# Performance work log

Measured on AMD Instinct MI355X. Metric: run time of the kernel, lower is better.

## Reference

```python
import jax, jax.numpy as jnp
import numpy as np
import math

M, INPUT_DIM, CLASSES, LATENT = 4096, 64, 10, 2

# ---- Bessel-approximation phi functions (Abramowitz & Stegun polynomial series) ----

def phi_f(s):
    t = s / 7.5
    t2 = t * t
    poly = 1.0 + 3.5156229 * t2 + 3.0899424 * t2**2 + 1.2067492 * t2**3 \
         + 0.2659732 * t2**4 + 0.0360768 * t2**5 + 0.0045813 * t2**6
    return jnp.exp(-s / 2.0) * poly


def phi_g(s):
    t = s / 7.5
    u = 1.0 / t  # s >= 7.5 when called via phi, so t >= 1
    poly = 0.39894228 + 0.01328592 * u + 0.00225319 * u**2 - 0.00157565 * u**3 \
         + 0.0091628 * u**4 - 0.02057706 * u**5 + 0.02635537 * u**6 \
         - 0.01647633 * u**7 + 0.00392377 * u**8
    return jnp.sqrt(2.0 / s) * poly


def phi(x):
    a = jnp.float32(7.5)
    return phi_f(jnp.minimum(x, a)) - phi_f(a) + phi_g(jnp.maximum(x, a))


def phi_d(s, D):
    if D <= 2:
        return phi(s)
    return 1.0 / jnp.sqrt(1.0 + 4.0 * s / (2 * D - 3))


def cramer_wold_distance(X, mu, variance, p, gamma):
    m, K = X.shape
    variance_matrix = variance[None, :] + variance[:, None]          # [C, C]
    # A term: pairwise latent-sample distances [m, m]
    A1 = jnp.sum((X[None, :, :] - X[:, None, :]) ** 2, axis=-1)      # [m, m]
    A = jnp.sum(phi_d(A1 / (4.0 * gamma), K)) / (m * m * math.sqrt(2.0 * math.pi * 2.0 * gamma))
    # B term: sample-to-mean distances [m, C]
    B1 = jnp.sum((mu[None, :, :] - X[:, None, :]) ** 2, axis=-1)     # [m, C]
    B2 = phi_d(B1 / (2.0 * (variance + 2.0 * gamma)), K)
    B = jnp.sum(2.0 * p / (m * jnp.sqrt(2.0 * math.pi * (variance + 2.0 * gamma))) * B2)
    # C term: mean-to-mean distances [C, C]
    C1 = jnp.sum((mu[None, :, :] - mu[:, None, :]) ** 2, axis=-1)
    C2 = phi_d(C1 / (2.0 * variance_matrix + 4.0 * gamma), K)
    C3 = jnp.outer(p, p) / jnp.sqrt(2.0 * math.pi * (variance_matrix + 2.0 * gamma))
    C = jnp.sum(C3 * C2)
    return A - B + C


def setup_inputs() -> dict:
    key = jax.random.key(0)
    ks = jax.random.split(key, 12)
    tau = jax.random.normal(ks[0], (M, INPUT_DIM), dtype=jnp.float32)
    # first half of batch is labeled (one-hot), second half unlabeled (zeros)
    lab_idx = jax.random.randint(ks[1], (M // 2,), 0, CLASSES)
    labels = jnp.concatenate([jax.nn.one_hot(lab_idx, CLASSES, dtype=jnp.float32),
                              jnp.zeros((M - M // 2, CLASSES), jnp.float32)], axis=0)
    batch_data = jnp.concatenate([tau, labels], axis=1)

    def xavier(k, fan_in, fan_out):
        lim = math.sqrt(6.0 / (fan_in + fan_out))
        return jax.random.uniform(k, (fan_in, fan_out), jnp.float32, -lim, lim)

    inp = {
        'batch_data': batch_data,
        'We1': xavier(ks[2], INPUT_DIM, 32), 'be1': jnp.zeros((32,), jnp.float32),
        'We2': xavier(ks[3], 32, 16),        'be2': jnp.zeros((16,), jnp.float32),
        'We3': xavier(ks[4], 16, LATENT),    'be3': jnp.zeros((LATENT,), jnp.float32),
        'Wd1': xavier(ks[5], LATENT, 16),    'bd1': jnp.zeros((16,), jnp.float32),
        'Wd2': xavier(ks[6], 16, 32),        'bd2': jnp.zeros((32,), jnp.float32),
        'Wd3': xavier(ks[7], 32, INPUT_DIM), 'bd3': jnp.zeros((INPUT_DIM,), jnp.float32),
        # GMM: init=2.0, gauss_num <= z_dim branch not taken (10 > 2) -> N(0, init)
        'means': 2.0 * jax.random.normal(ks[8], (CLASSES, LATENT), jnp.float32),
        'variances': jnp.ones((CLASSES,), jnp.float32),
        'probs': jnp.full((CLASSES,), 1.0 / CLASSES, jnp.float32),
    }
    return inp


def segma_forward(batch_data, We1, be1, We2, be2, We3, be3,
                  Wd1, bd1, Wd2, bd2, Wd3, bd3, means, variances, probs):
    tau = batch_data[:, :INPUT_DIM]
    labels = batch_data[:, INPUT_DIM:]
    # encoder
    x = jnp.tanh(tau @ We1 + be1)
    x = jnp.tanh(x @ We2 + be2)
    z = x @ We3 + be3                                               # [m, K]
    # decoder
    h = jnp.tanh(z @ Wd1 + bd1)
    h = jnp.tanh(h @ Wd2 + bd2)
    tau_decoded = h @ Wd3 + bd3
    rec_loss = jnp.mean((tau - tau_decoded) ** 2)
    # labeled mask: rows whose one-hot labels sum to exactly 1
    labeled_mask = (jnp.sum(labels, axis=-1) == 1.0)
    # class logits: Gaussian log-likelihood under each mixture component
    D = means.shape[-1]
    sq = jnp.sum((z[:, None, :] - means[None, :, :]) ** 2, axis=-1)  # [m, C]
    class_logits = jnp.log(probs) - 0.5 * D * jnp.log(2.0 * math.pi * variances) - sq / (2.0 * variances)
    # cross-entropy with (soft/one-hot) float targets, masked to labeled rows
    ce = -jnp.sum(labels * jax.nn.log_softmax(class_logits, axis=-1), axis=-1)
    den = jnp.sum(labels)
    den = jnp.where(den == 0, 1.0, den)
    class_loss = jnp.sum(ce * labeled_mask.astype(jnp.float32)) / den
    # Cramer-Wold cost (train_labeled=True -> use all z)
    m = z.shape[0]
    gamma = jnp.float32((4.0 / (3.0 * m)) ** 0.2)
    cw_cost = cramer_wold_distance(z, means, variances, probs, gamma)
    log_cw_cost = 8.0 + jnp.log(cw_cost)
    total_loss = rec_loss + 1.0 * log_cw_cost + 2.0 * class_loss
    return total_loss


def reference(batch_data, We1, be1, We2, be2, We3, be3,
              Wd1, bd1, Wd2, bd2, Wd3, bd3, means, variances, probs):
    return segma_forward(batch_data, We1, be1, We2, be2, We3, be3,
                         Wd1, bd1, Wd2, bd2, Wd3, bd3, means, variances, probs)
```

## Files before the change

kernel.cpp:

```cpp
#include <hip/hip_runtime.h>
#include <math.h>

#define M_ROWS 4096
#define IN_DIM 64
#define NCLS 10
#define ROW_STRIDE 74
#define TWO_PI_F 6.283185307179586f

__device__ __forceinline__ float phi_f_eval(float s) {
    float t = s * (1.0f / 7.5f);
    float t2 = t * t;
    float p = 0.0045813f;
    p = fmaf(p, t2, 0.0360768f);
    p = fmaf(p, t2, 0.2659732f);
    p = fmaf(p, t2, 1.2067492f);
    p = fmaf(p, t2, 3.0899424f);
    p = fmaf(p, t2, 3.5156229f);
    p = fmaf(p, t2, 1.0f);
    return __expf(-0.5f * s) * p;
}

__device__ __forceinline__ float phi_g_eval(float s) {
    float r = __builtin_amdgcn_rcpf(s);
    float u = 7.5f * r;
    float p = 0.00392377f;
    p = fmaf(p, u, -0.01647633f);
    p = fmaf(p, u, 0.02635537f);
    p = fmaf(p, u, -0.02057706f);
    p = fmaf(p, u, 0.0091628f);
    p = fmaf(p, u, -0.00157565f);
    p = fmaf(p, u, 0.00225319f);
    p = fmaf(p, u, 0.01328592f);
    p = fmaf(p, u, 0.39894228f);
    return __builtin_amdgcn_sqrtf(2.0f * r) * p;
}

#define PHI_F_75 0.21445709f

__device__ __forceinline__ float phi_eval(float s) {
    float f = phi_f_eval(fminf(s, 7.5f));
    float g = phi_g_eval(fmaxf(s, 7.5f));
    return f - PHI_F_75 + g;
}

__device__ __forceinline__ float fast_tanh(float x) {
    float e = __expf(2.0f * x);
    float r = __builtin_amdgcn_rcpf(e + 1.0f);
    return fmaf(-2.0f, r, 1.0f);
}

__device__ __forceinline__ float waveReduce(float v) {
    v += __shfl_down(v, 32, 64);
    v += __shfl_down(v, 16, 64);
    v += __shfl_down(v, 8, 64);
    v += __shfl_down(v, 4, 64);
    v += __shfl_down(v, 2, 64);
    v += __shfl_down(v, 1, 64);
    return v;
}

#define O_W1T   0
#define O_W2T   2048
#define O_WD2T  2560
#define O_WD3T  3072
#define O_W3T   5120
#define O_WD1T  5152
#define O_B1    5184
#define O_B2    5216
#define O_B3    5232
#define O_BD1   5236
#define O_BD2   5252
#define O_BD3   5284
#define O_MU    5348
#define O_VAR   5368
#define O_PRB   5378
#define SM_TOT  5392

__global__ __launch_bounds__(64, 1) void k_mlp(
    const float* __restrict__ batch,
    const float* __restrict__ We1, const float* __restrict__ be1,
    const float* __restrict__ We2, const float* __restrict__ be2,
    const float* __restrict__ We3, const float* __restrict__ be3,
    const float* __restrict__ Wd1, const float* __restrict__ bd1,
    const float* __restrict__ Wd2, const float* __restrict__ bd2,
    const float* __restrict__ Wd3, const float* __restrict__ bd3,
    const float* __restrict__ means, const float* __restrict__ vars,
    const float* __restrict__ probs,
    float2* __restrict__ zbuf,
    float* __restrict__ recp, float* __restrict__ Bp,
    float* __restrict__ clsp, float* __restrict__ labp,
    float gamma)
{
    __shared__ __align__(16) float sm[SM_TOT];
    const int tid = threadIdx.x;

    for (int idx = tid; idx < 2048; idx += 64) { int i = idx >> 5, j = idx & 31; sm[O_W1T + j * 64 + i] = We1[idx]; }
    for (int idx = tid; idx < 512;  idx += 64) { int i = idx >> 4, j = idx & 15; sm[O_W2T + j * 32 + i] = We2[idx]; }
    for (int idx = tid; idx < 512;  idx += 64) { int i = idx >> 5, j = idx & 31; sm[O_WD2T + j * 16 + i] = Wd2[idx]; }
    for (int idx = tid; idx < 2048; idx += 64) { int i = idx >> 6, j = idx & 63; sm[O_WD3T + j * 32 + i] = Wd3[idx]; }
    if (tid < 32) { int i = tid >> 1, j = tid & 1;  sm[O_W3T + j * 16 + i] = We3[tid]; }
    else          { int t2 = tid - 32; int i = t2 >> 4, j = t2 & 15; sm[O_WD1T + j * 2 + i] = Wd1[t2]; }
    if (tid < 32) sm[O_B1 + tid] = be1[tid];
    if (tid < 16) sm[O_B2 + tid] = be2[tid];
    if (tid < 2)  sm[O_B3 + tid] = be3[tid];
    if (tid < 16) sm[O_BD1 + tid] = bd1[tid];
    if (tid < 32) sm[O_BD2 + tid] = bd2[tid];
    {
        sm[O_BD3 + tid] = bd3[tid];
    }
    if (tid < 20) sm[O_MU + tid] = means[tid];
    if (tid < 10) sm[O_VAR + tid] = vars[tid];
    if (tid < 10) sm[O_PRB + tid] = probs[tid];
    __syncthreads();

    const int row = blockIdx.x * 64 + tid;
    const float* rp = batch + (size_t)row * ROW_STRIDE;

    float tau[64];
#pragma unroll
    for (int i = 0; i < 32; i++) {
        float2 v = ((const float2*)rp)[i];
        tau[2 * i] = v.x; tau[2 * i + 1] = v.y;
    }

    float x1[32];
#pragma unroll
    for (int j = 0; j < 32; j++) {
        const float4* w = (const float4*)&sm[O_W1T + j * 64];
        float acc = sm[O_B1 + j];
#pragma unroll
        for (int i = 0; i < 16; i++) {
            float4 wv = w[i];
            acc = fmaf(tau[4 * i],     wv.x, acc);
            acc = fmaf(tau[4 * i + 1], wv.y, acc);
            acc = fmaf(tau[4 * i + 2], wv.z, acc);
            acc = fmaf(tau[4 * i + 3], wv.w, acc);
        }
        x1[j] = fast_tanh(acc);
    }

    float x2[16];
#pragma unroll
    for (int j = 0; j < 16; j++) {
        const float4* w = (const float4*)&sm[O_W2T + j * 32];
        float acc = sm[O_B2 + j];
#pragma unroll
        for (int i = 0; i < 8; i++) {
            float4 wv = w[i];
            acc = fmaf(x1[4 * i],     wv.x, acc);
            acc = fmaf(x1[4 * i + 1], wv.y, acc);
            acc = fmaf(x1[4 * i + 2], wv.z, acc);
            acc = fmaf(x1[4 * i + 3], wv.w, acc);
        }
        x2[j] = fast_tanh(acc);
    }

    float z0 = sm[O_B3 + 0], z1 = sm[O_B3 + 1];
#pragma unroll
    for (int i = 0; i < 16; i++) {
        z0 = fmaf(x2[i], sm[O_W3T + 0 * 16 + i], z0);
        z1 = fmaf(x2[i], sm[O_W3T + 1 * 16 + i], z1);
    }
    zbuf[row] = make_float2(z0, z1);

    float h1[16];
#pragma unroll
    for (int j = 0; j < 16; j++) {
        float acc = sm[O_BD1 + j];
        acc = fmaf(z0, sm[O_WD1T + j * 2 + 0], acc);
        acc = fmaf(z1, sm[O_WD1T + j * 2 + 1], acc);
        h1[j] = fast_tanh(acc);
    }

    float h2[32];
#pragma unroll
    for (int j = 0; j < 32; j++) {
        const float4* w = (const float4*)&sm[O_WD2T + j * 16];
        float acc = sm[O_BD2 + j];
#pragma unroll
        for (int i = 0; i < 4; i++) {
            float4 wv = w[i];
            acc = fmaf(h1[4 * i],     wv.x, acc);
            acc = fmaf(h1[4 * i + 1], wv.y, acc);
            acc = fmaf(h1[4 * i + 2], wv.z, acc);
            acc = fmaf(h1[4 * i + 3], wv.w, acc);
        }
        h2[j] = fast_tanh(acc);
    }

    float rec = 0.0f;
#pragma unroll
    for (int o = 0; o < 64; o++) {
        const float4* w = (const float4*)&sm[O_WD3T + o * 32];
        float acc = sm[O_BD3 + o];
#pragma unroll
        for (int i = 0; i < 8; i++) {
            float4 wv = w[i];
            acc = fmaf(h2[4 * i],     wv.x, acc);
            acc = fmaf(h2[4 * i + 1], wv.y, acc);
            acc = fmaf(h2[4 * i + 2], wv.z, acc);
            acc = fmaf(h2[4 * i + 3], wv.w, acc);
        }
        float e = acc - tau[o];
        rec = fmaf(e, e, rec);
    }

    const float two_g = 2.0f * gamma;
    const float inv_m = 1.0f / (float)M_ROWS;
    float lg[NCLS];
    float mx = -3.0e38f;
    float Bacc = 0.0f;
#pragma unroll
    for (int c = 0; c < NCLS; c++) {
        float d0 = z0 - sm[O_MU + 2 * c];
        float d1 = z1 - sm[O_MU + 2 * c + 1];
        float sqc = fmaf(d0, d0, d1 * d1);
        float vc = sm[O_VAR + c];
        float lgc = __logf(sm[O_PRB + c]) - __logf(TWO_PI_F * vc)
                    - sqc * 0.5f * __builtin_amdgcn_rcpf(vc);
        lg[c] = lgc;
        mx = fmaxf(mx, lgc);

        float den = vc + two_g;
        float sB = sqc * 0.5f * __builtin_amdgcn_rcpf(den);
        float coef = 2.0f * inv_m * sm[O_PRB + c] * __builtin_amdgcn_rsqf(TWO_PI_F * den);
        Bacc = fmaf(coef, phi_eval(sB), Bacc);
    }
    float esum = 0.0f;
#pragma unroll
    for (int c = 0; c < NCLS; c++) esum += __expf(lg[c] - mx);
    float lse = __logf(esum) + mx;

    float suml = 0.0f, ce = 0.0f;
#pragma unroll
    for (int c = 0; c < NCLS; c++) {
        float lb = rp[IN_DIM + c];
        suml += lb;
        ce = fmaf(lb, lse - lg[c], ce);
    }
    float cls = (suml == 1.0f) ? ce : 0.0f;

    float r0 = waveReduce(rec);
    float r1 = waveReduce(Bacc);
    float r2 = waveReduce(cls);
    float r3 = waveReduce(suml);
    if (tid == 0) {
        recp[blockIdx.x] = r0;
        Bp[blockIdx.x]   = r1;
        clsp[blockIdx.x] = r2;
        labp[blockIdx.x] = r3;
    }
}

__global__ __launch_bounds__(64, 1) void k_pair(
    const float2* __restrict__ z, float* __restrict__ Apart, float inv4g)
{
    const int ti = blockIdx.x, tj = blockIdx.y;
    const int bid = blockIdx.x + gridDim.x * blockIdx.y;
    const int lane = threadIdx.x;
    if (tj < ti) {
        if (lane == 0) Apart[bid] = 0.0f;
        return;
    }
    __shared__ float2 zjs[64];
    const int i = ti * 64 + lane;
    float2 zi = z[i];
    zjs[lane] = z[tj * 64 + lane];
    __syncthreads();

    const bool offd = (ti != tj);
    float acc = 0.0f;
#pragma unroll 8
    for (int jj = 0; jj < 64; jj++) {
        float dx = zi.x - zjs[jj].x;
        float dy = zi.y - zjs[jj].y;
        float s = fmaf(dx, dx, dy * dy) * inv4g;
        float p = phi_eval(s);
        if (offd || (tj * 64 + jj) > i) acc += p;
    }
    float tot = waveReduce(acc);
    if (lane == 0) Apart[bid] = tot;
}

__global__ __launch_bounds__(256) void k_fin(
    const float* __restrict__ means, const float* __restrict__ vars,
    const float* __restrict__ probs,
    const float* __restrict__ Apart,
    const float* __restrict__ recp, const float* __restrict__ Bp,
    const float* __restrict__ clsp, const float* __restrict__ labp,
    float* __restrict__ out, float gamma)
{
    __shared__ double sA[256];
    __shared__ double s4[256];
    __shared__ float cbuf[256];
    const int t = threadIdx.x;

    float cval = 0.0f;
    if (t < 100) {
        int ci = t / 10, cj = t - 10 * (t / 10);
        float vm = vars[ci] + vars[cj];
        float d0 = means[2 * ci] - means[2 * cj];
        float d1 = means[2 * ci + 1] - means[2 * cj + 1];
        float c1 = fmaf(d0, d0, d1 * d1);
        float s = c1 / (2.0f * vm + 4.0f * gamma);
        float c2 = phi_eval(s);
        float c3 = probs[ci] * probs[cj] * __builtin_amdgcn_rsqf(TWO_PI_F * (vm + 2.0f * gamma));
        cval = c3 * c2;
    }
    cbuf[t] = cval;

    double av = 0.0;
#pragma unroll
    for (int k = 0; k < 16; k++) av += (double)Apart[t + 256 * k];
    sA[t] = av;

    double pv;
    if (t < 64)       pv = (double)recp[t];
    else if (t < 128) pv = (double)Bp[t - 64];
    else if (t < 192) pv = (double)clsp[t - 128];
    else              pv = (double)labp[t - 192];
    s4[t] = pv;
    __syncthreads();

    if (t == 0) {
        double Asum = 0.0, C = 0.0, rec = 0.0, B = 0.0, cls = 0.0, lab = 0.0;
        for (int k = 0; k < 256; k++) Asum += sA[k];
        for (int k = 0; k < 256; k++) C += (double)cbuf[k];
        for (int k = 0; k < 64; k++)  rec += s4[k];
        for (int k = 64; k < 128; k++) B += s4[k];
        for (int k = 128; k < 192; k++) cls += s4[k];
        for (int k = 192; k < 256; k++) lab += s4[k];

        const double m = (double)M_ROWS;
        const double gam = (double)gamma;
        double phi0 = (double)phi_eval(0.0f);
        double Atot = 2.0 * Asum + m * phi0;
        double A = Atot / (m * m * sqrt(2.0 * M_PI * 2.0 * gam));
        double den = lab; if (den == 0.0) den = 1.0;
        double cw = A - B + C;
        double total = rec / (m * 64.0) + 8.0 + log(cw) + 2.0 * (cls / den);
        out[0] = (float)total;
    }
}

extern "C" void kernel_launch(void* const* d_in, const int* in_sizes, int n_in,
                              void* d_out, int out_size, void* d_ws, size_t ws_size,
                              hipStream_t stream) {
    (void)in_sizes; (void)n_in; (void)out_size; (void)ws_size;
    const float* batch = (const float*)d_in[0];
    const float* We1 = (const float*)d_in[1];
    const float* be1 = (const float*)d_in[2];
    const float* We2 = (const float*)d_in[3];
    const float* be2 = (const float*)d_in[4];
    const float* We3 = (const float*)d_in[5];
    const float* be3 = (const float*)d_in[6];
    const float* Wd1 = (const float*)d_in[7];
    const float* bd1 = (const float*)d_in[8];
    const float* Wd2 = (const float*)d_in[9];
    const float* bd2 = (const float*)d_in[10];
    const float* Wd3 = (const float*)d_in[11];
    const float* bd3 = (const float*)d_in[12];
    const float* means = (const float*)d_in[13];
    const float* vars = (const float*)d_in[14];
    const float* probs = (const float*)d_in[15];

    float* ws = (float*)d_ws;
    float2* zbuf = (float2*)ws;
    float* Apart = ws + 8192;
    float* recp  = ws + 12288;
    float* Bp    = ws + 12352;
    float* clsp  = ws + 12416;
    float* labp  = ws + 12480;

    const float gamma = (float)pow(4.0 / (3.0 * (double)M_ROWS), 0.2);
    const float inv4g = 1.0f / (4.0f * gamma);

    k_mlp<<<64, 64, 0, stream>>>(batch, We1, be1, We2, be2, We3, be3,
                                 Wd1, bd1, Wd2, bd2, Wd3, bd3,
                                 means, vars, probs,
                                 zbuf, recp, Bp, clsp, labp, gamma);
    k_pair<<<dim3(64, 64), 64, 0, stream>>>(zbuf, Apart, inv4g);
    k_fin<<<1, 256, 0, stream>>>(means, vars, probs, Apart, recp, Bp, clsp, labp,
                                 (float*)d_out, gamma);
}
```

Measured before the change: 140.7 us.

## Launch only upper-triangular pair tiles and parallelize final reduction with wave shuffles

```diff
diff --git a/kernel.cpp b/kernel.cpp
--- a/kernel.cpp
+++ b/kernel.cpp
@@ -6,6 +6,8 @@
 #define NCLS 10
 #define ROW_STRIDE 74
 #define TWO_PI_F 6.283185307179586f
+#define NTILE 64
+#define NPAIR 2080
 
 __device__ __forceinline__ float phi_f_eval(float s) {
     float t = s * (1.0f / 7.5f);
@@ -50,6 +52,16 @@
 }
 
 __device__ __forceinline__ float waveReduce(float v) {
+    v += __shfl_down(v, 32, 64);
+    v += __shfl_down(v, 16, 64);
+    v += __shfl_down(v, 8, 64);
+    v += __shfl_down(v, 4, 64);
+    v += __shfl_down(v, 2, 64);
+    v += __shfl_down(v, 1, 64);
+    return v;
+}
+
+__device__ __forceinline__ double waveReduceD(double v) {
     v += __shfl_down(v, 32, 64);
     v += __shfl_down(v, 16, 64);
     v += __shfl_down(v, 8, 64);
@@ -105,9 +117,7 @@
     if (tid < 2)  sm[O_B3 + tid] = be3[tid];
     if (tid < 16) sm[O_BD1 + tid] = bd1[tid];
     if (tid < 32) sm[O_BD2 + tid] = bd2[tid];
-    {
-        sm[O_BD3 + tid] = bd3[tid];
-    }
+    sm[O_BD3 + tid] = bd3[tid];
     if (tid < 20) sm[O_MU + tid] = means[tid];
     if (tid < 10) sm[O_VAR + tid] = vars[tid];
     if (tid < 10) sm[O_PRB + tid] = probs[tid];
@@ -252,34 +262,32 @@
     }
 }
 
-__global__ __launch_bounds__(64, 1) void k_pair(
+__global__ __launch_bounds__(64, 4) void k_pair(
     const float2* __restrict__ z, float* __restrict__ Apart, float inv4g)
 {
-    const int ti = blockIdx.x, tj = blockIdx.y;
-    const int bid = blockIdx.x + gridDim.x * blockIdx.y;
+    const int p = blockIdx.x;
+    int tj = (int)((__builtin_amdgcn_sqrtf(8.0f * (float)p + 1.0f) - 1.0f) * 0.5f);
+    while ((tj + 1) * (tj + 2) / 2 <= p) tj++;
+    while (tj * (tj + 1) / 2 > p) tj--;
+    const int ti = p - tj * (tj + 1) / 2;
+
     const int lane = threadIdx.x;
-    if (tj < ti) {
-        if (lane == 0) Apart[bid] = 0.0f;
-        return;
-    }
     __shared__ float2 zjs[64];
-    const int i = ti * 64 + lane;
-    float2 zi = z[i];
+    float2 zi = z[ti * 64 + lane];
     zjs[lane] = z[tj * 64 + lane];
     __syncthreads();
 
-    const bool offd = (ti != tj);
-    float acc = 0.0f;
+    float acc0 = 0.0f, acc1 = 0.0f;
 #pragma unroll 8
-    for (int jj = 0; jj < 64; jj++) {
-        float dx = zi.x - zjs[jj].x;
-        float dy = zi.y - zjs[jj].y;
-        float s = fmaf(dx, dx, dy * dy) * inv4g;
-        float p = phi_eval(s);
-        if (offd || (tj * 64 + jj) > i) acc += p;
-    }
-    float tot = waveReduce(acc);
-    if (lane == 0) Apart[bid] = tot;
+    for (int jj = 0; jj < 64; jj += 2) {
+        float2 a = zjs[jj], b = zjs[jj + 1];
+        float dx0 = zi.x - a.x, dy0 = zi.y - a.y;
+        float dx1 = zi.x - b.x, dy1 = zi.y - b.y;
+        acc0 += phi_eval(fmaf(dx0, dx0, dy0 * dy0) * inv4g);
+        acc1 += phi_eval(fmaf(dx1, dx1, dy1 * dy1) * inv4g);
+    }
+    float tot = waveReduce(acc0 + acc1);
+    if (lane == 0) Apart[p] = (ti == tj) ? tot : 2.0f * tot;
 }
 
 __global__ __launch_bounds__(256) void k_fin(
@@ -290,12 +298,22 @@
     const float* __restrict__ clsp, const float* __restrict__ labp,
     float* __restrict__ out, float gamma)
 {
-    __shared__ double sA[256];
-    __shared__ double s4[256];
-    __shared__ float cbuf[256];
+    __shared__ double wsum[8];
     const int t = threadIdx.x;
-
-    float cval = 0.0f;
+    const int w = t >> 6;
+
+    const double m = (double)M_ROWS;
+    const double gam = (double)gamma;
+    const double invA = 1.0 / (m * m * sqrt(2.0 * M_PI * 2.0 * gam));
+
+    double av = 0.0;
+#pragma unroll
+    for (int k = 0; k < 9; k++) {
+        int idx = t + 256 * k;
+        if (idx < NPAIR) av += (double)Apart[idx];
+    }
+
+    double cv = 0.0;
     if (t < 100) {
         int ci = t / 10, cj = t - 10 * (t / 10);
         float vm = vars[ci] + vars[cj];
@@ -305,39 +323,27 @@
         float s = c1 / (2.0f * vm + 4.0f * gamma);
         float c2 = phi_eval(s);
         float c3 = probs[ci] * probs[cj] * __builtin_amdgcn_rsqf(TWO_PI_F * (vm + 2.0f * gamma));
-        cval = c3 * c2;
-    }
-    cbuf[t] = cval;
-
-    double av = 0.0;
-#pragma unroll
-    for (int k = 0; k < 16; k++) av += (double)Apart[t + 256 * k];
-    sA[t] = av;
-
+        cv = (double)(c3 * c2);
+    }
+
+    double acw = waveReduceD(av * invA + cv);
+
+    const int l = t & 63;
     double pv;
-    if (t < 64)       pv = (double)recp[t];
-    else if (t < 128) pv = (double)Bp[t - 64];
-    else if (t < 192) pv = (double)clsp[t - 128];
-    else              pv = (double)labp[t - 192];
-    s4[t] = pv;
+    if (w == 0)      pv = (double)recp[l];
+    else if (w == 1) pv = (double)Bp[l];
+    else if (w == 2) pv = (double)clsp[l];
+    else             pv = (double)labp[l];
+    double pw = waveReduceD(pv);
+
+    if (l == 0) { wsum[w] = acw; wsum[4 + w] = pw; }
     __syncthreads();
 
     if (t == 0) {
-        double Asum = 0.0, C = 0.0, rec = 0.0, B = 0.0, cls = 0.0, lab = 0.0;
-        for (int k = 0; k < 256; k++) Asum += sA[k];
-        for (int k = 0; k < 256; k++) C += (double)cbuf[k];
-        for (int k = 0; k < 64; k++)  rec += s4[k];
-        for (int k = 64; k < 128; k++) B += s4[k];
-        for (int k = 128; k < 192; k++) cls += s4[k];
-        for (int k = 192; k < 256; k++) lab += s4[k];
-
-        const double m = (double)M_ROWS;
-        const double gam = (double)gamma;
-        double phi0 = (double)phi_eval(0.0f);
-        double Atot = 2.0 * Asum + m * phi0;
-        double A = Atot / (m * m * sqrt(2.0 * M_PI * 2.0 * gam));
-        double den = lab; if (den == 0.0) den = 1.0;
-        double cw = A - B + C;
+        double AC = wsum[0] + wsum[1] + wsum[2] + wsum[3];
+        double rec = wsum[4], B = wsum[5], cls = wsum[6], lab = wsum[7];
+        double den = (lab == 0.0) ? 1.0 : lab;
+        double cw = AC - B;
         double total = rec / (m * 64.0) + 8.0 + log(cw) + 2.0 * (cls / den);
         out[0] = (float)total;
     }
@@ -379,7 +385,7 @@
                                  Wd1, bd1, Wd2, bd2, Wd3, bd3,
                                  means, vars, probs,
                                  zbuf, recp, Bp, clsp, labp, gamma);
-    k_pair<<<dim3(64, 64), 64, 0, stream>>>(zbuf, Apart, inv4g);
+    k_pair<<<NPAIR, 64, 0, stream>>>(zbuf, Apart, inv4g);
     k_fin<<<1, 256, 0, stream>>>(means, vars, probs, Apart, recp, Bp, clsp, labp,
                                  (float*)d_out, gamma);
 }
```

Measured after the change: 131.4 us. 6.6% less time.
